# Kernel optimization log

Measured on AMD Instinct MI355X. Metric: run time of the kernel, lower is better.

The kernel has to match this reference:

```python
import jax, jax.numpy as jnp
import numpy as np

N = 100000
E = 1_600_000
EPS = 1e-5
NEG_SLOPE = 0.01


def leaky_relu(x):
    return jnp.where(x > 0, x, NEG_SLOPE * x)


def batchnorm(x, gamma, beta):
    # BatchNorm1d in training mode: batch statistics, biased variance
    m = jnp.mean(x, axis=0)
    v = jnp.mean((x - m) ** 2, axis=0)
    return (x - m) * jax.lax.rsqrt(v + EPS) * gamma + beta


def gcn_conv(x, W, b, src, dst, norm, n):
    # PyG GCNConv: h = x @ W; aggregate norm * h[src] into dst; add bias
    h = x @ W                              # [N, F_out]
    msgs = h[src] * norm[:, None]          # [E', F_out] gather + scale
    out = jax.ops.segment_sum(msgs, dst, num_segments=n)  # scatter-add
    return out + b


def setup_inputs() -> dict:
    key = jax.random.key(0)
    ks = jax.random.split(key, 14)
    d_in, d_h1, d_h2, d_out = 128, 128, 64, 8
    x = jax.random.normal(ks[0], (N, d_in), dtype=jnp.float32)
    edge_index = jax.random.randint(ks[1], (2, E), 0, N, dtype=jnp.int64)
    edge_weights = jax.random.uniform(ks[2], (E,), dtype=jnp.float32)
    # Glorot-ish init for GCNConv weights, zero bias (PyG default bias=True)
    W1 = jax.random.normal(ks[3], (d_in, d_h1), dtype=jnp.float32) / np.sqrt(d_in)
    b1 = jnp.zeros((d_h1,), jnp.float32)
    W2 = jax.random.normal(ks[4], (d_h1, d_h2), dtype=jnp.float32) / np.sqrt(d_h1)
    b2 = jnp.zeros((d_h2,), jnp.float32)
    W3 = jax.random.normal(ks[5], (d_h2, d_out), dtype=jnp.float32) / np.sqrt(d_h2)
    b3 = jnp.zeros((d_out,), jnp.float32)
    gamma1 = jnp.ones((d_h1,), jnp.float32)
    beta1 = jnp.zeros((d_h1,), jnp.float32)
    gamma2 = jnp.ones((d_h2,), jnp.float32)
    beta2 = jnp.zeros((d_h2,), jnp.float32)
    return {"x": x, "edge_index": edge_index, "edge_weights": edge_weights,
            "W1": W1, "b1": b1, "W2": W2, "b2": b2, "W3": W3, "b3": b3,
            "gamma1": gamma1, "beta1": beta1, "gamma2": gamma2, "beta2": beta2}


def reference(x, edge_index, edge_weights, W1, b1, W2, b2, W3, b3,
              gamma1, beta1, gamma2, beta2):
    # edge_weights is accepted (as in the original forward signature) but unused:
    # the module calls GCNConv(x, edge_index) without weights.
    n = x.shape[0]
    loop = jnp.arange(n, dtype=edge_index.dtype)
    src = jnp.concatenate([edge_index[0], loop])  # add self-loops
    dst = jnp.concatenate([edge_index[1], loop])
    # symmetric normalization with unit edge weights (in-degree on dst)
    deg = jax.ops.segment_sum(jnp.ones_like(dst, dtype=x.dtype), dst,
                              num_segments=n)
    dinv = jnp.where(deg > 0, jax.lax.rsqrt(deg), 0.0)
    norm = dinv[src] * dinv[dst]

    h = leaky_relu(gcn_conv(x, W1, b1, src, dst, norm, n))
    h = batchnorm(h, gamma1, beta1)
    h = leaky_relu(gcn_conv(h, W2, b2, src, dst, norm, n))
    h = batchnorm(h, gamma2, beta2)
    h = leaky_relu(gcn_conv(h, W3, b3, src, dst, norm, n))
    return h
```

## Files before the change

kernel.cpp:

```cpp
#include <hip/hip_runtime.h>
#include <cstdint>
#include <cstddef>

#define NEG_SLOPE 0.01f
#define BN_EPS 1e-5f
#define BSHIFT 6
#define BMASK 63
#define NBLK 128

using short8 = __attribute__((ext_vector_type(8))) short;
using f32x4 = __attribute__((ext_vector_type(4))) float;

__device__ inline unsigned short f2bf(float f) {
    unsigned int u = __float_as_uint(f);
    u += 0x7FFFu + ((u >> 16) & 1u);
    return (unsigned short)(u >> 16);
}


__global__ __launch_bounds__(1024) void pre_kernel(const int* __restrict__ dst,
                                                   int* __restrict__ hist,
                                                   int E, int nb, int chunk,
                                                   const float* __restrict__ W1,
                                                   unsigned short* __restrict__ wt1,
                                                   const float* __restrict__ W2,
                                                   unsigned short* __restrict__ wt2) {
    const int b = blockIdx.x;
    if (b < NBLK) {
        __shared__ int lh[2048];
        for (int i = threadIdx.x; i < nb; i += 1024) lh[i] = 0;
        __syncthreads();
        const int e0 = b * chunk;
        const int e1 = min(E, e0 + chunk);
        for (int e = e0 + threadIdx.x; e < e1; e += 1024)
            atomicAdd(&lh[dst[e] >> BSHIFT], 1);
        __syncthreads();
        for (int k = threadIdx.x; k < nb; k += 1024)
            hist[k * NBLK + b] = lh[k];
    } else {
        int idx = (b - NBLK) * 1024 + threadIdx.x;
        if (idx < 128 * 128) {
            int k = idx >> 7, n = idx & 127;
            wt1[n * 128 + k] = f2bf(W1[idx]);
        } else if (idx < 128 * 128 + 128 * 64) {
            int j = idx - 128 * 128;
            int k = j >> 6, n = j & 63;
            wt2[n * 128 + k] = f2bf(W2[j]);
        }
    }
}

__global__ __launch_bounds__(1024) void scan_block_kernel(const int* __restrict__ in,
                                                          int* __restrict__ out,
                                                          int* __restrict__ partials, int n) {
    __shared__ int sm[1024];
    int tid = threadIdx.x;
    int i = blockIdx.x * 1024 + tid;
    int v = (i < n) ? in[i] : 0;
    int x = v;
    sm[tid] = x;
    __syncthreads();
    for (int off = 1; off < 1024; off <<= 1) {
        int y = (tid >= off) ? sm[tid - off] : 0;
        __syncthreads();
        x += y;
        sm[tid] = x;
        __syncthreads();
    }
    if (i < n) out[i] = x - v;
    if (tid == 1023) partials[blockIdx.x] = x;
}

__global__ __launch_bounds__(1024) void chunkscatter_kernel(const int* __restrict__ src,
                                                            const int* __restrict__ dst,
                                                            const int* __restrict__ S,
                                                            const int* __restrict__ partials,
                                                            unsigned int* __restrict__ packed,
                                                            int E, int nb, int chunk, int MB) {
    __shared__ int cur[2048];
    __shared__ int pof[256];
    const int b = blockIdx.x;
    if (threadIdx.x == 0) {
        int acc = 0;
        for (int i = 0; i < MB; ++i) { pof[i] = acc; acc += partials[i]; }
    }
    __syncthreads();
    for (int k = threadIdx.x; k < nb; k += 1024) {
        const int i = k * NBLK + b;
        cur[k] = S[i] + pof[i >> 10];
    }
    __syncthreads();
    const int e0 = b * chunk;
    const int e1 = min(E, e0 + chunk);
    for (int e = e0 + threadIdx.x; e < e1; e += 1024) {
        int d = dst[e];
        int slot = atomicAdd(&cur[d >> BSHIFT], 1);
        packed[slot] = ((unsigned int)src[e] << BSHIFT) | (unsigned int)(d & BMASK);
    }
}

__global__ __launch_bounds__(256) void bucket_build_kernel(const unsigned int* __restrict__ packed,
                                                           const int* __restrict__ S,
                                                           const int* __restrict__ partials,
                                                           int* __restrict__ rowptr,
                                                           float* __restrict__ dinv,
                                                           int* __restrict__ csr,
                                                           int N, int nb, int E, int MB) {
    const int b = blockIdx.x;
    const int t = threadIdx.x;
    __shared__ int pof[256];
    __shared__ int eb[2];
    if (t == 0) {
        int acc = 0;
        for (int i = 0; i < MB; ++i) { pof[i] = acc; acc += partials[i]; }
        const int i0 = b * NBLK;
        eb[0] = S[i0] + pof[i0 >> 10];
        if (b == nb - 1) eb[1] = E;
        else {
            const int i1 = (b + 1) * NBLK;
            eb[1] = S[i1] + pof[i1 >> 10];
        }
    }
    __syncthreads();
    const int e0 = eb[0], e1 = eb[1];
    const int node0 = b << BSHIFT;
    __shared__ int h2[1024];
    __shared__ int tsum[256];
    for (int i = t; i < 1024; i += 256) h2[i] = 0;
    __syncthreads();
    for (int e = e0 + t; e < e1; e += 256) {
        const unsigned int p = packed[e];
        const int ldst = p & BMASK;
        int s4 = (int)(p >> BSHIFT) >> 13;
        if (s4 > 15) s4 = 15;
        atomicAdd(&h2[(ldst << 4) | s4], 1);
    }
    __syncthreads();
    const int v0 = h2[4 * t], v1 = h2[4 * t + 1], v2 = h2[4 * t + 2], v3 = h2[4 * t + 3];
    const int tot = v0 + v1 + v2 + v3;
    int x = tot;
    tsum[t] = x;
    __syncthreads();
    for (int o = 1; o < 256; o <<= 1) {
        int y = (t >= o) ? tsum[t - o] : 0;
        __syncthreads();
        x += y;
        tsum[t] = x;
        __syncthreads();
    }
    const int base = e0 + x - tot;
    h2[4 * t] = base;
    h2[4 * t + 1] = base + v0;
    h2[4 * t + 2] = base + v0 + v1;
    h2[4 * t + 3] = base + v0 + v1 + v2;
    __syncthreads();
    if (t < 64) {
        const int gs = h2[t << 4];
        const int ge = (t == 63) ? e1 : h2[(t + 1) << 4];
        const int node = node0 + t;
        if (node < N) {
            rowptr[node] = gs;
            dinv[node] = rsqrtf((float)(ge - gs + 1));
        }
    }
    if (b == nb - 1 && t == 0) rowptr[N] = E;
    __syncthreads();
    for (int e = e0 + t; e < e1; e += 256) {
        const unsigned int p = packed[e];
        const int ldst = p & BMASK;
        const int src = (int)(p >> BSHIFT);
        int s4 = src >> 13;
        if (s4 > 15) s4 = 15;
        const int slot = atomicAdd(&h2[(ldst << 4) | s4], 1);
        csr[slot] = src;
    }
}


template <int MF, bool BN, bool XBF>
__global__ __launch_bounds__(256) void mgemm_kernel(const void* __restrict__ Xv,
                                                    const unsigned short* __restrict__ Wt,
                                                    const float* __restrict__ bnS,
                                                    const float* __restrict__ bnT,
                                                    const float* __restrict__ dinv,
                                                    unsigned short* __restrict__ H, int n) {
    constexpr int K = 128;
    constexpr int CTW = (MF / 16) / 4;
    __shared__ unsigned short Xl[64 * K];
    __shared__ unsigned short Wl[MF * K];
    __shared__ float dl[64];

    const int t = threadIdx.x;
    const int wave = t >> 6;
    const int lane = t & 63;
    const int row0 = blockIdx.x * 64;

    if (XBF) {
        const unsigned short* X = (const unsigned short*)Xv;
        for (int idx = t; idx < 64 * K / 8; idx += 256) {
            int r = idx >> 4, c8 = idx & 15;
            int row = row0 + r; if (row >= n) row = n - 1;
            uint4 v = ((const uint4*)(X + (size_t)row * K))[c8];
            float xv[8];
            xv[0] = __uint_as_float(v.x << 16); xv[1] = __uint_as_float(v.x & 0xFFFF0000u);
            xv[2] = __uint_as_float(v.y << 16); xv[3] = __uint_as_float(v.y & 0xFFFF0000u);
            xv[4] = __uint_as_float(v.z << 16); xv[5] = __uint_as_float(v.z & 0xFFFF0000u);
            xv[6] = __uint_as_float(v.w << 16); xv[7] = __uint_as_float(v.w & 0xFFFF0000u);
            if (BN) {
                const float4 s0 = ((const float4*)bnS)[c8 * 2];
                const float4 s1 = ((const float4*)bnS)[c8 * 2 + 1];
                const float4 t0 = ((const float4*)bnT)[c8 * 2];
                const float4 t1 = ((const float4*)bnT)[c8 * 2 + 1];
                xv[0] = xv[0] * s0.x + t0.x; xv[1] = xv[1] * s0.y + t0.y;
                xv[2] = xv[2] * s0.z + t0.z; xv[3] = xv[3] * s0.w + t0.w;
                xv[4] = xv[4] * s1.x + t1.x; xv[5] = xv[5] * s1.y + t1.y;
                xv[6] = xv[6] * s1.z + t1.z; xv[7] = xv[7] * s1.w + t1.w;
            }
            uint4 o;
            o.x = (unsigned)f2bf(xv[0]) | ((unsigned)f2bf(xv[1]) << 16);
            o.y = (unsigned)f2bf(xv[2]) | ((unsigned)f2bf(xv[3]) << 16);
            o.z = (unsigned)f2bf(xv[4]) | ((unsigned)f2bf(xv[5]) << 16);
            o.w = (unsigned)f2bf(xv[6]) | ((unsigned)f2bf(xv[7]) << 16);
            *(uint4*)((char*)Xl + r * 256 + ((c8 * 16) ^ ((r & 7) << 4))) = o;
        }
    } else {
        const float* X = (const float*)Xv;
        for (int idx = t; idx < 64 * K / 4; idx += 256) {
            int r = idx >> 5, c4 = idx & 31;
            int row = row0 + r; if (row >= n) row = n - 1;
            float4 v = ((const float4*)(X + (size_t)row * K))[c4];
            if (BN) {
                float4 sv = ((const float4*)bnS)[c4];
                float4 tv = ((const float4*)bnT)[c4];
                v.x = v.x * sv.x + tv.x; v.y = v.y * sv.y + tv.y;
                v.z = v.z * sv.z + tv.z; v.w = v.w * sv.w + tv.w;
            }
            ushort4 o; o.x = f2bf(v.x); o.y = f2bf(v.y); o.z = f2bf(v.z); o.w = f2bf(v.w);
            *(ushort4*)((char*)Xl + r * 256 + ((c4 * 8) ^ ((r & 7) << 4))) = o;
        }
    }
    for (int idx = t; idx < MF * K / 4; idx += 256) {
        int nr = idx >> 5, k4 = idx & 31;
        ushort4 o = ((const ushort4*)(Wt + (size_t)nr * K))[k4];
        *(ushort4*)((char*)Wl + nr * 256 + ((k4 * 8) ^ ((nr & 7) << 4))) = o;
    }
    if (t < 64) { int row = row0 + t; dl[t] = dinv[row < n ? row : n - 1]; }
    __syncthreads();

    f32x4 acc[CTW][4];
#pragma unroll
    for (int c = 0; c < CTW; ++c)
#pragma unroll
        for (int rt = 0; rt < 4; ++rt)
            acc[c][rt] = (f32x4){0.f, 0.f, 0.f, 0.f};

    const int kg = lane >> 4;
    const int lr = lane & 15;

#pragma unroll
    for (int kk = 0; kk < 4; ++kk) {
        const int kb = (kk * 32 + kg * 8) * 2;
        short8 a[4];
#pragma unroll
        for (int rt = 0; rt < 4; ++rt) {
            int r = rt * 16 + lr;
            a[rt] = *(const short8*)((const char*)Xl + r * 256 + (kb ^ ((r & 7) << 4)));
        }
#pragma unroll
        for (int c = 0; c < CTW; ++c) {
            int nr = (wave * CTW + c) * 16 + lr;
            short8 b = *(const short8*)((const char*)Wl + nr * 256 + (kb ^ ((nr & 7) << 4)));
#pragma unroll
            for (int rt = 0; rt < 4; ++rt)
                acc[c][rt] = __builtin_amdgcn_mfma_f32_16x16x32_bf16(a[rt], b, acc[c][rt], 0, 0, 0);
        }
    }
    __syncthreads();

    unsigned short* Ol = (unsigned short*)Xl;
#pragma unroll
    for (int c = 0; c < CTW; ++c) {
        int col = (wave * CTW + c) * 16 + lr;
#pragma unroll
        for (int rt = 0; rt < 4; ++rt) {
#pragma unroll
            for (int j = 0; j < 4; ++j) {
                int r = rt * 16 + kg * 4 + j;
                Ol[r * MF + col] = f2bf(acc[c][rt][j] * dl[r]);
            }
        }
    }
    __syncthreads();
    for (int idx = t; idx < 64 * MF / 4; idx += 256) {
        int r = idx / (MF / 4), c4 = idx % (MF / 4);
        int row = row0 + r;
        if (row < n)
            ((ushort4*)(H + (size_t)row * MF))[c4] = ((const ushort4*)Ol)[idx];
    }
}


__global__ __launch_bounds__(256) void gemm3_kernel(const unsigned short* __restrict__ X,
                                                    const float* __restrict__ W,
                                                    const float* __restrict__ bnS,
                                                    const float* __restrict__ bnT,
                                                    const float* __restrict__ dinv,
                                                    unsigned short* __restrict__ H, int n) {
    __shared__ float Wl[512];
    __shared__ float sl[64], tl[64];
    const int t = threadIdx.x;
    for (int i = t; i < 512; i += 256) Wl[i] = W[i];
    if (t < 64) { sl[t] = bnS[t]; tl[t] = bnT[t]; }
    __syncthreads();
    const int node = blockIdx.x * 256 + t;
    if (node >= n) return;
    float acc[8];
#pragma unroll
    for (int m = 0; m < 8; ++m) acc[m] = 0.f;
    const uint4* xp = (const uint4*)(X + (size_t)node * 64);
#pragma unroll
    for (int c8 = 0; c8 < 8; ++c8) {
        const uint4 v = xp[c8];
        float xv[8];
        xv[0] = __uint_as_float(v.x << 16); xv[1] = __uint_as_float(v.x & 0xFFFF0000u);
        xv[2] = __uint_as_float(v.y << 16); xv[3] = __uint_as_float(v.y & 0xFFFF0000u);
        xv[4] = __uint_as_float(v.z << 16); xv[5] = __uint_as_float(v.z & 0xFFFF0000u);
        xv[6] = __uint_as_float(v.w << 16); xv[7] = __uint_as_float(v.w & 0xFFFF0000u);
#pragma unroll
        for (int j = 0; j < 8; ++j) {
            const int k = c8 * 8 + j;
            const float x = xv[j] * sl[k] + tl[k];
#pragma unroll
            for (int m = 0; m < 8; ++m) acc[m] += x * Wl[k * 8 + m];
        }
    }
    const float di = dinv[node];
    uint4 o;
    o.x = (unsigned)f2bf(acc[0] * di) | ((unsigned)f2bf(acc[1] * di) << 16);
    o.y = (unsigned)f2bf(acc[2] * di) | ((unsigned)f2bf(acc[3] * di) << 16);
    o.z = (unsigned)f2bf(acc[4] * di) | ((unsigned)f2bf(acc[5] * di) << 16);
    o.w = (unsigned)f2bf(acc[6] * di) | ((unsigned)f2bf(acc[7] * di) << 16);
    *(uint4*)(H + (size_t)node * 8) = o;
}


template <int F, int GROUP, bool BF16OUT>
__global__ __launch_bounds__(256) void agg_kernel(const unsigned short* __restrict__ h,
                                                  const int* __restrict__ rowptr,
                                                  const int* __restrict__ csr,
                                                  const float* __restrict__ dinv,
                                                  const float* __restrict__ bias,
                                                  void* __restrict__ yout, int n) {
    constexpr int NPB = 256 / GROUP;
    const int g = threadIdx.x % GROUP;
    const int node = blockIdx.x * NPB + threadIdx.x / GROUP;
    if (node >= n) return;
    const int f0 = g * 8;
    const unsigned short* hp = h + f0;
    float a0 = 0.f, a1 = 0.f, a2 = 0.f, a3 = 0.f, a4 = 0.f, a5 = 0.f, a6 = 0.f, a7 = 0.f;
#define ACC8(v)                                    \
    a0 += __uint_as_float((v).x << 16);            \
    a1 += __uint_as_float((v).x & 0xFFFF0000u);    \
    a2 += __uint_as_float((v).y << 16);            \
    a3 += __uint_as_float((v).y & 0xFFFF0000u);    \
    a4 += __uint_as_float((v).z << 16);            \
    a5 += __uint_as_float((v).z & 0xFFFF0000u);    \
    a6 += __uint_as_float((v).w << 16);            \
    a7 += __uint_as_float((v).w & 0xFFFF0000u);
    int e = rowptr[node];
    const int r1 = rowptr[node + 1];
    for (; e + 4 <= r1; e += 4) {
        const int s0 = csr[e], s1 = csr[e + 1], s2 = csr[e + 2], s3 = csr[e + 3];
        const uint4 v0 = *(const uint4*)(hp + (size_t)s0 * F);
        const uint4 v1 = *(const uint4*)(hp + (size_t)s1 * F);
        const uint4 v2 = *(const uint4*)(hp + (size_t)s2 * F);
        const uint4 v3 = *(const uint4*)(hp + (size_t)s3 * F);
        ACC8(v0); ACC8(v1); ACC8(v2); ACC8(v3);
    }
    for (; e < r1; ++e) {
        const int s = csr[e];
        const uint4 v = *(const uint4*)(hp + (size_t)s * F);
        ACC8(v);
    }
    {
        const uint4 v = *(const uint4*)(hp + (size_t)node * F);
        ACC8(v);
    }
#undef ACC8
    const float di = dinv[node];
    const float4 bA = *(const float4*)(bias + f0);
    const float4 bB = *(const float4*)(bias + f0 + 4);
    float r[8];
    r[0] = di * a0 + bA.x; r[1] = di * a1 + bA.y;
    r[2] = di * a2 + bA.z; r[3] = di * a3 + bA.w;
    r[4] = di * a4 + bB.x; r[5] = di * a5 + bB.y;
    r[6] = di * a6 + bB.z; r[7] = di * a7 + bB.w;
#pragma unroll
    for (int k = 0; k < 8; ++k) r[k] = r[k] > 0.f ? r[k] : NEG_SLOPE * r[k];
    if (BF16OUT) {
        uint4 o;
        o.x = (unsigned)f2bf(r[0]) | ((unsigned)f2bf(r[1]) << 16);
        o.y = (unsigned)f2bf(r[2]) | ((unsigned)f2bf(r[3]) << 16);
        o.z = (unsigned)f2bf(r[4]) | ((unsigned)f2bf(r[5]) << 16);
        o.w = (unsigned)f2bf(r[6]) | ((unsigned)f2bf(r[7]) << 16);
        *(uint4*)((unsigned short*)yout + (size_t)node * F + f0) = o;
    } else {
        float4 o0, o1;
        o0.x = r[0]; o0.y = r[1]; o0.z = r[2]; o0.w = r[3];
        o1.x = r[4]; o1.y = r[5]; o1.z = r[6]; o1.w = r[7];
        float* yp = (float*)yout + (size_t)node * F + f0;
        *(float4*)(yp) = o0;
        *(float4*)(yp + 4) = o1;
    }
}


template <int F>
__global__ __launch_bounds__(256) void bstats_kernel(const unsigned short* __restrict__ y,
                                                     float* __restrict__ sumP,
                                                     float* __restrict__ ssqP,
                                                     int n, int nblocks) {
    constexpr int GROUP = F / 8;
    constexpr int NPB = 256 / GROUP;
    const int g = threadIdx.x % GROUP;
    const int slot = threadIdx.x / GROUP;
    const int f0 = g * 8;
    float ss[8], qq[8];
#pragma unroll
    for (int k = 0; k < 8; ++k) { ss[k] = 0.f; qq[k] = 0.f; }
    for (int base = blockIdx.x * NPB; base < n; base += nblocks * NPB) {
        const int node = base + slot;
        if (node < n) {
            const uint4 v = *(const uint4*)(y + (size_t)node * F + f0);
            float xv[8];
            xv[0] = __uint_as_float(v.x << 16); xv[1] = __uint_as_float(v.x & 0xFFFF0000u);
            xv[2] = __uint_as_float(v.y << 16); xv[3] = __uint_as_float(v.y & 0xFFFF0000u);
            xv[4] = __uint_as_float(v.z << 16); xv[5] = __uint_as_float(v.z & 0xFFFF0000u);
            xv[6] = __uint_as_float(v.w << 16); xv[7] = __uint_as_float(v.w & 0xFFFF0000u);
#pragma unroll
            for (int k = 0; k < 8; ++k) { ss[k] += xv[k]; qq[k] += xv[k] * xv[k]; }
        }
    }
    __shared__ float smS[F], smQ[F];
    for (int i = threadIdx.x; i < F; i += 256) { smS[i] = 0.f; smQ[i] = 0.f; }
    __syncthreads();
#pragma unroll
    for (int k = 0; k < 8; ++k) {
        atomicAdd(&smS[f0 + k], ss[k]);
        atomicAdd(&smQ[f0 + k], qq[k]);
    }
    __syncthreads();
    for (int i = threadIdx.x; i < F; i += 256) {
        sumP[(size_t)blockIdx.x * F + i] = smS[i];
        ssqP[(size_t)blockIdx.x * F + i] = smQ[i];
    }
}


__global__ __launch_bounds__(256) void bnparam_kernel(const float* __restrict__ sumP,
                                                      const float* __restrict__ ssqP,
                                                      const float* __restrict__ gamma,
                                                      const float* __restrict__ beta,
                                                      float* __restrict__ S, float* __restrict__ T,
                                                      int n, int F, int NB) {
    const int f = blockIdx.x;
    const int t = threadIdx.x;
    float s = 0.f, q = 0.f;
    for (int b = t; b < NB; b += 256) {
        s += sumP[(size_t)b * F + f];
        q += ssqP[(size_t)b * F + f];
    }
    __shared__ float rs[4], rq[4];
    for (int o = 32; o; o >>= 1) { s += __shfl_down(s, o); q += __shfl_down(q, o); }
    if ((t & 63) == 0) { rs[t >> 6] = s; rq[t >> 6] = q; }
    __syncthreads();
    if (t == 0) {
        s = rs[0] + rs[1] + rs[2] + rs[3];
        q = rq[0] + rq[1] + rq[2] + rq[3];
        const float m = s / (float)n;
        const float var = q / (float)n - m * m;
        const float inv = rsqrtf(var + BN_EPS);
        const float sc = gamma[f] * inv;
        S[f] = sc;
        T[f] = beta[f] - m * sc;
    }
}


extern "C" void kernel_launch(void* const* d_in, const int* in_sizes, int n_in,
                              void* d_out, int out_size, void* d_ws, size_t ws_size,
                              hipStream_t stream) {
    const float* x = (const float*)d_in[0];
    const int* edges = (const int*)d_in[1];
    const float* W1 = (const float*)d_in[3];
    const float* b1 = (const float*)d_in[4];
    const float* W2 = (const float*)d_in[5];
    const float* b2 = (const float*)d_in[6];
    const float* W3 = (const float*)d_in[7];
    const float* b3 = (const float*)d_in[8];
    const float* gamma1 = (const float*)d_in[9];
    const float* beta1 = (const float*)d_in[10];
    const float* gamma2 = (const float*)d_in[11];
    const float* beta2 = (const float*)d_in[12];

    const int N = in_sizes[0] / 128;
    const int E = in_sizes[1] / 2;
    const int* esrc = edges;
    const int* edst = edges + E;
    const int nb = (N + BMASK) >> BSHIFT;
    const int M = nb * NBLK;
    const int chunk = (E + NBLK - 1) / NBLK;
    const int NBS = 1024;

    char* ws = (char*)d_ws;
    size_t off = 0;
    auto alloc = [&](size_t bytes) -> void* {
        void* p = ws + off;
        off = (off + bytes + 255) & ~(size_t)255;
        return p;
    };
    int* hist = (int*)alloc((size_t)M * 4);
    int* S = (int*)alloc((size_t)M * 4);
    int* partials = (int*)alloc(1024 * 4);
    int* rowptr = (int*)alloc((size_t)(N + 1) * 4);
    float* dinv = (float*)alloc((size_t)N * 4);
    float* bn = (float*)alloc(512 * 4);
    float* sumP1 = (float*)alloc((size_t)NBS * 128 * 4);
    float* ssqP1 = (float*)alloc((size_t)NBS * 128 * 4);
    float* sumP2 = (float*)alloc((size_t)NBS * 64 * 4);
    float* ssqP2 = (float*)alloc((size_t)NBS * 64 * 4);
    unsigned short* wt1 = (unsigned short*)alloc(128 * 128 * 2);
    unsigned short* wt2 = (unsigned short*)alloc(64 * 128 * 2);
    int* csr = (int*)alloc((size_t)E * 4);
    unsigned short* hbuf = (unsigned short*)alloc((size_t)N * 128 * 2);
    unsigned short* ybuf = (unsigned short*)alloc((size_t)N * 128 * 2);
    unsigned int* packed = (unsigned int*)hbuf;

    float* sA = bn;
    float* tA = bn + 128;
    float* sB = bn + 256;
    float* tB = bn + 384;

    const int MB = (M + 1023) / 1024;
    const int TBLK = (128 * 128 + 128 * 64 + 1023) / 1024;

    pre_kernel<<<NBLK + TBLK, 1024, 0, stream>>>(edst, hist, E, nb, chunk, W1, wt1, W2, wt2);
    scan_block_kernel<<<MB, 1024, 0, stream>>>(hist, S, partials, M);
    chunkscatter_kernel<<<NBLK, 1024, 0, stream>>>(esrc, edst, S, partials, packed, E, nb, chunk, MB);
    bucket_build_kernel<<<nb, 256, 0, stream>>>(packed, S, partials, rowptr, dinv, csr, N, nb, E, MB);

    mgemm_kernel<128, false, false><<<(N + 63) / 64, 256, 0, stream>>>(x, wt1, nullptr, nullptr, dinv, hbuf, N);
    agg_kernel<128, 16, true><<<(N + 15) / 16, 256, 0, stream>>>(hbuf, rowptr, csr, dinv, b1, ybuf, N);
    bstats_kernel<128><<<NBS, 256, 0, stream>>>(ybuf, sumP1, ssqP1, N, NBS);
    bnparam_kernel<<<128, 256, 0, stream>>>(sumP1, ssqP1, gamma1, beta1, sA, tA, N, 128, NBS);

    mgemm_kernel<64, true, true><<<(N + 63) / 64, 256, 0, stream>>>(ybuf, wt2, sA, tA, dinv, hbuf, N);
    agg_kernel<64, 8, true><<<(N + 31) / 32, 256, 0, stream>>>(hbuf, rowptr, csr, dinv, b2, ybuf, N);
    bstats_kernel<64><<<NBS, 256, 0, stream>>>(ybuf, sumP2, ssqP2, N, NBS);
    bnparam_kernel<<<64, 256, 0, stream>>>(sumP2, ssqP2, gamma2, beta2, sB, tB, N, 64, NBS);

    gemm3_kernel<<<(N + 255) / 256, 256, 0, stream>>>(ybuf, W3, sB, tB, dinv, hbuf, N);
    agg_kernel<8, 1, false><<<(N + 255) / 256, 256, 0, stream>>>(hbuf, rowptr, csr, dinv, b3, (float*)d_out, N);
}
```

Measured before the change: 267.3 us.

## Double scatter block count and parallelize partial-offset prefix scans

Raises NBLK from 128 to 256 so the edge scatter uses more blocks, each handling a smaller chunk, which spreads the atomic-heavy bucket scatter across more CUs. With more blocks the number of scan partials (MB) grows, so the serial single-thread prefix over partials in the chunkscatter and bucket_build kernels is replaced with block-wide parallel scans. The parallel scans add several barriers per block, and the larger histogram (nb*NBLK) increases the preceding scan work.

```diff
diff --git a/kernel.cpp b/kernel.cpp
--- a/kernel.cpp
+++ b/kernel.cpp
@@ -6,7 +6,7 @@
 #define BN_EPS 1e-5f
 #define BSHIFT 6
 #define BMASK 63
-#define NBLK 128
+#define NBLK 256
 
 using short8 = __attribute__((ext_vector_type(8))) short;
 using f32x4 = __attribute__((ext_vector_type(4))) float;
@@ -78,21 +78,32 @@
                                                             unsigned int* __restrict__ packed,
                                                             int E, int nb, int chunk, int MB) {
     __shared__ int cur[2048];
-    __shared__ int pof[256];
+    __shared__ int pof[1024];
     const int b = blockIdx.x;
-    if (threadIdx.x == 0) {
-        int acc = 0;
-        for (int i = 0; i < MB; ++i) { pof[i] = acc; acc += partials[i]; }
-    }
-    __syncthreads();
-    for (int k = threadIdx.x; k < nb; k += 1024) {
+    const int t = threadIdx.x;
+    {
+        const int v = (t < MB) ? partials[t] : 0;
+        int x = v;
+        pof[t] = x;
+        __syncthreads();
+        for (int o = 1; o < 1024; o <<= 1) {
+            int y = (t >= o) ? pof[t - o] : 0;
+            __syncthreads();
+            x += y;
+            pof[t] = x;
+            __syncthreads();
+        }
+        pof[t] = x - v;
+        __syncthreads();
+    }
+    for (int k = t; k < nb; k += 1024) {
         const int i = k * NBLK + b;
         cur[k] = S[i] + pof[i >> 10];
     }
     __syncthreads();
     const int e0 = b * chunk;
     const int e1 = min(E, e0 + chunk);
-    for (int e = e0 + threadIdx.x; e < e1; e += 1024) {
+    for (int e = e0 + t; e < e1; e += 1024) {
         int d = dst[e];
         int slot = atomicAdd(&cur[d >> BSHIFT], 1);
         packed[slot] = ((unsigned int)src[e] << BSHIFT) | (unsigned int)(d & BMASK);
@@ -108,24 +119,46 @@
                                                            int N, int nb, int E, int MB) {
     const int b = blockIdx.x;
     const int t = threadIdx.x;
-    __shared__ int pof[256];
+    __shared__ int pofS[1024];
+    __shared__ int tsum[256];
     __shared__ int eb[2];
+    {
+        const int b4 = t * 4;
+        const int v0 = (b4     < MB) ? partials[b4]     : 0;
+        const int v1 = (b4 + 1 < MB) ? partials[b4 + 1] : 0;
+        const int v2 = (b4 + 2 < MB) ? partials[b4 + 2] : 0;
+        const int v3 = (b4 + 3 < MB) ? partials[b4 + 3] : 0;
+        const int s = v0 + v1 + v2 + v3;
+        int x = s;
+        tsum[t] = x;
+        __syncthreads();
+        for (int o = 1; o < 256; o <<= 1) {
+            int y = (t >= o) ? tsum[t - o] : 0;
+            __syncthreads();
+            x += y;
+            tsum[t] = x;
+            __syncthreads();
+        }
+        const int excl = x - s;
+        pofS[b4] = excl;
+        pofS[b4 + 1] = excl + v0;
+        pofS[b4 + 2] = excl + v0 + v1;
+        pofS[b4 + 3] = excl + v0 + v1 + v2;
+        __syncthreads();
+    }
     if (t == 0) {
-        int acc = 0;
-        for (int i = 0; i < MB; ++i) { pof[i] = acc; acc += partials[i]; }
         const int i0 = b * NBLK;
-        eb[0] = S[i0] + pof[i0 >> 10];
+        eb[0] = S[i0] + pofS[i0 >> 10];
         if (b == nb - 1) eb[1] = E;
         else {
             const int i1 = (b + 1) * NBLK;
-            eb[1] = S[i1] + pof[i1 >> 10];
+            eb[1] = S[i1] + pofS[i1 >> 10];
         }
     }
     __syncthreads();
     const int e0 = eb[0], e1 = eb[1];
     const int node0 = b << BSHIFT;
     __shared__ int h2[1024];
-    __shared__ int tsum[256];
     for (int i = t; i < 1024; i += 256) h2[i] = 0;
     __syncthreads();
     for (int e = e0 + t; e < e1; e += 256) {
```

Result: faster. 261.0 us (-2.4%).
